# Kernel optimization log

Hardware: AMD Instinct MI355X
Metric: run time of the kernel (lower is better)

Reference implementation:

```python
import jax, jax.numpy as jnp
import numpy as np

# norse-default LIF/LI constants (RecNet overrides alpha=80, tau_mem_inv=100)
DT = 0.001
ALPHA = 80.0
TAU_SYN_INV = 200.0   # 1/5e-3 (default)
TAU_MEM_INV = 100.0   # 1/0.01 (passed explicitly)
V_TH, V_RESET, V_LEAK = 1.0, 0.0, 0.0

@jax.custom_vjp
def superspike(x):
    # heaviside forward, SuperSpike surrogate backward
    return (x > 0).astype(x.dtype)

def _ss_fwd(x):
    return (x > 0).astype(x.dtype), x

def _ss_bwd(x, g):
    return (g / (ALPHA * jnp.abs(x) + 1.0) ** 2,)

superspike.defvjp(_ss_fwd, _ss_bwd)

def setup_inputs() -> dict:
    key = jax.random.key(0)
    k1, k2, k3, k4 = jax.random.split(key, 4)
    T, B, F, H, O = 100, 512, 784, 512, 10
    x = jax.random.normal(k1, (T, B, 1, 28, 28), dtype=jnp.float32)
    w_in = jax.random.normal(k2, (H, F), dtype=jnp.float32) / np.sqrt(F)
    w_rec = jax.random.normal(k3, (H, H), dtype=jnp.float32) / np.sqrt(H)
    w_out = jax.random.normal(k4, (O, H), dtype=jnp.float32) / np.sqrt(H)
    return {"x": x, "w_in": w_in, "w_rec": w_rec, "w_out": w_out}

def reference(x, w_in, w_rec, w_out):
    T, B = x.shape[0], x.shape[1]
    Hd = w_in.shape[0]
    Od = w_out.shape[0]
    xf = x.reshape(T, B, -1)  # [T, B, F]

    z0 = jnp.zeros((B, Hd), x.dtype)
    lv0 = jnp.zeros((B, Od), x.dtype)
    init = (z0, z0, z0, lv0, lv0)  # (z, v, i, li_v, li_i)

    def step(carry, xt):
        z, v, i, lv, li = carry
        # LIF recurrent cell (norse lif_step)
        v_dec = v + DT * TAU_MEM_INV * ((V_LEAK - v) + i)
        i_dec = i - DT * TAU_SYN_INV * i
        z_new = superspike(v_dec - V_TH)
        v_new = (1.0 - z_new) * v_dec + z_new * V_RESET
        i_new = i_dec + xt @ w_in.T + z @ w_rec.T  # previous z for recurrence
        # readout linear (no bias)
        y = z_new @ w_out.T
        # LI cell (norse li_feed_forward_step): vo uses old current
        lv_new = lv + DT * TAU_MEM_INV * ((V_LEAK - lv) + li)
        li_new = li - DT * TAU_SYN_INV * li + y
        return (z_new, v_new, i_new, lv_new, li_new), lv_new

    _, voltages = jax.lax.scan(step, init, xf)
    return voltages  # [T, B, O]
```

## Files before the change

### kernel.cpp

```cpp
#include <hip/hip_runtime.h>


#define TT    100
#define BATCH 512
#define FDIM  784
#define HDIM  512
#define ODIM  10
#define NSTATE (BATCH * HDIM)

#define DTM 0.1
#define DTS 0.2

__global__ __launch_bounds__(256) void gemm_in_kernel(const float* __restrict__ A,
                                                      const float* __restrict__ B,
                                                      double* __restrict__ C) {
  __shared__ double As[16][130];
  __shared__ double Bs[16][66];
  const int tid = threadIdx.x;
  const int tn = tid & 15;
  const int tm = tid >> 4;
  const int m0 = blockIdx.x << 7;
  const int n0 = blockIdx.y << 6;

  double acc[8][4] = {};

  for (int kt = 0; kt < 49; ++kt) {
    __syncthreads();
#pragma unroll
    for (int s = 0; s < 2; ++s) {
      const int idx = tid + (s << 8);
      const int row = idx >> 2;
      const int kc  = (idx & 3) << 2;
      const float4 a = *(const float4*)(A + (size_t)(m0 + row) * FDIM + kt * 16 + kc);
      As[kc + 0][row] = (double)a.x; As[kc + 1][row] = (double)a.y;
      As[kc + 2][row] = (double)a.z; As[kc + 3][row] = (double)a.w;
    }
    {
      const int row = tid >> 2;
      const int kc  = (tid & 3) << 2;
      const float4 b = *(const float4*)(B + (size_t)(n0 + row) * FDIM + kt * 16 + kc);
      Bs[kc + 0][row] = (double)b.x; Bs[kc + 1][row] = (double)b.y;
      Bs[kc + 2][row] = (double)b.z; Bs[kc + 3][row] = (double)b.w;
    }
    __syncthreads();
#pragma unroll
    for (int kk = 0; kk < 16; ++kk) {
      double av[8], bv[4];
      *(double2*)&av[0] = *(const double2*)&As[kk][(tm << 3) + 0];
      *(double2*)&av[2] = *(const double2*)&As[kk][(tm << 3) + 2];
      *(double2*)&av[4] = *(const double2*)&As[kk][(tm << 3) + 4];
      *(double2*)&av[6] = *(const double2*)&As[kk][(tm << 3) + 6];
      *(double2*)&bv[0] = *(const double2*)&Bs[kk][(tn << 2) + 0];
      *(double2*)&bv[2] = *(const double2*)&Bs[kk][(tn << 2) + 2];
#pragma unroll
      for (int i = 0; i < 8; ++i)
#pragma unroll
        for (int j = 0; j < 4; ++j) acc[i][j] += av[i] * bv[j];
    }
  }
#pragma unroll
  for (int i = 0; i < 8; ++i) {
    double* crow = C + (size_t)(m0 + (tm << 3) + i) * HDIM + n0 + (tn << 2);
    *(double2*)(crow)     = make_double2(acc[i][0], acc[i][1]);
    *(double2*)(crow + 2) = make_double2(acc[i][2], acc[i][3]);
  }
}

__global__ __launch_bounds__(256) void transpose_kernel(const float* __restrict__ src,
                                                        float* __restrict__ dst) {
  __shared__ float tile[32][33];
  const int bx = blockIdx.x & 15, by = blockIdx.x >> 4;
  const int tx = threadIdx.x & 31, ty = threadIdx.x >> 5;
  const int x = (bx << 5) + tx;
#pragma unroll
  for (int s = 0; s < 32; s += 8)
    tile[ty + s][tx] = src[(size_t)((by << 5) + ty + s) * HDIM + x];
  __syncthreads();
  const int xo = (by << 5) + tx;
#pragma unroll
  for (int s = 0; s < 32; s += 8)
    dst[(size_t)((bx << 5) + ty + s) * HDIM + xo] = tile[tx][ty + s];
}

__global__ __launch_bounds__(256) void wot_kernel(const float* __restrict__ w_out,
                                                  float* __restrict__ wot) {
  const int k = (blockIdx.x << 8) + threadIdx.x;
#pragma unroll
  for (int o = 0; o < ODIM; ++o) wot[(k << 4) + o] = w_out[(size_t)o * HDIM + k];
}

__global__ __launch_bounds__(256) void lif_kernel(const double* __restrict__ cin,
                                                  const float* __restrict__ wrt,
                                                  const float* __restrict__ wot,
                                                  float* __restrict__ out) {
  const int b = blockIdx.x;
  const int tid = threadIdx.x;
  const int h0 = tid, h1 = tid + 256;

  __shared__ unsigned long long masks[8];
  __shared__ int offs[9];
  __shared__ __align__(8) unsigned short list[528];
  __shared__ double ypart[256];

  if (tid == 0) offs[8] = 0;
  __syncthreads();

  double v0 = 0.0, v1 = 0.0, i0 = 0.0, i1 = 0.0;
  double lv = 0.0, li = 0.0;

  const double* cinb = cin + (size_t)b * HDIM;
  float* outb = out + (size_t)b * ODIM;

  for (int t = 0; t < TT; ++t) {
    const double vd0 = v0 + DTM * ((0.0 - v0) + i0);
    const double vd1 = v1 + DTM * ((0.0 - v1) + i1);
    const bool s0 = (vd0 - 1.0) > 0.0;
    const bool s1 = (vd1 - 1.0) > 0.0;
    v0 = s0 ? 0.0 : vd0;
    v1 = s1 ? 0.0 : vd1;
    i0 = i0 - DTS * i0;
    i1 = i1 - DTS * i1;

    const double c0 = cinb[(size_t)t * NSTATE + h0];
    const double c1 = cinb[(size_t)t * NSTATE + h1];

    {
      const int nf = offs[8];
      const int nfp = (nf + 3) & ~3;
      if (nfp > 0) {
        float A0[4], A1[4], B0[4] = {}, B1[4] = {};
#define LOADG(base, X0, X1)                                                   \
        do {                                                                  \
          const unsigned long long le = *(const unsigned long long*)&list[base]; \
          const int k0 = (int)(le & 0xffffu), k1 = (int)((le >> 16) & 0xffffu); \
          const int k2 = (int)((le >> 32) & 0xffffu), k3 = (int)(le >> 48);   \
          X0[0] = wrt[(k0 << 9) + h0]; X1[0] = wrt[(k0 << 9) + h1];           \
          X0[1] = wrt[(k1 << 9) + h0]; X1[1] = wrt[(k1 << 9) + h1];           \
          X0[2] = wrt[(k2 << 9) + h0]; X1[2] = wrt[(k2 << 9) + h1];           \
          X0[3] = wrt[(k3 << 9) + h0]; X1[3] = wrt[(k3 << 9) + h1];           \
        } while (0)
        LOADG(0, A0, A1);
        for (int g = 0; g < nfp; g += 4) {
          if (g + 4 < nfp) LOADG(g + 4, B0, B1);
          i0 += (double)A0[0]; i1 += (double)A1[0];
          i0 += (double)A0[1]; i1 += (double)A1[1];
          i0 += (double)A0[2]; i1 += (double)A1[2];
          i0 += (double)A0[3]; i1 += (double)A1[3];
#pragma unroll
          for (int j = 0; j < 4; ++j) { A0[j] = B0[j]; A1[j] = B1[j]; }
        }
#undef LOADG
      }
    }
    i0 += c0;
    i1 += c1;

    __syncthreads();

    {
      const unsigned long long m0 = __ballot(s0);
      const unsigned long long m1 = __ballot(s1);
      const int w = tid >> 6;
      if ((tid & 63) == 0) { masks[w] = m0; masks[4 + w] = m1; }
    }
    __syncthreads();
    if (tid == 0) {
      int r = 0;
#pragma unroll
      for (int q = 0; q < 8; ++q) { offs[q] = r; r += __popcll(masks[q]); }
      offs[8] = r;
    }
    __syncthreads();
    if (tid < 8) {
      unsigned long long m = masks[tid];
      int o = offs[tid];
      const int base = tid << 6;
      while (m) {
        list[o++] = (unsigned short)(base + __builtin_ctzll(m));
        m &= m - 1;
      }
    }
    if (tid < 4) list[offs[8] + tid] = 512;
    __syncthreads();

    {
      const int o = tid & 15, q = tid >> 4;
      const int nfc = offs[8];
      double yp = 0.0;
      int kk = q;
      if (kk < nfc) {
        float f = wot[((int)list[kk] << 4) + o];
        for (kk += 16; kk < nfc; kk += 16) {
          const float fn = wot[((int)list[kk] << 4) + o];
          yp += (double)f;
          f = fn;
        }
        yp += (double)f;
      }
      ypart[(o << 4) + q] = yp;
    }
    __syncthreads();
    if (tid < ODIM) {
      double y = 0.0;
      const double* yr = &ypart[tid << 4];
#pragma unroll
      for (int q = 0; q < 16; ++q) y += yr[q];
      const double lvn = lv + DTM * ((0.0 - lv) + li);
      li = (li - DTS * li) + y;
      lv = lvn;
      outb[(size_t)t * (BATCH * ODIM) + tid] = (float)lvn;
    }
  }
}

extern "C" void kernel_launch(void* const* d_in, const int* in_sizes, int n_in,
                              void* d_out, int out_size, void* d_ws, size_t ws_size,
                              hipStream_t stream) {
  const float* x     = (const float*)d_in[0];
  const float* w_in  = (const float*)d_in[1];
  const float* w_rec = (const float*)d_in[2];
  const float* w_out = (const float*)d_in[3];
  float* out = (float*)d_out;

  const size_t CIN = (size_t)TT * BATCH * HDIM;
  double* cin = (double*)d_ws;
  float* wrt = (float*)(cin + CIN);
  float* wot = wrt + 513 * 512;

  const size_t aux_floats = 513ull * 512 + 513ull * 16;
  const size_t need_bytes = CIN * sizeof(double) + aux_floats * sizeof(float);
  if (ws_size < need_bytes) {
    hipMemsetAsync(d_out, 0x7F, (size_t)out_size * sizeof(float), stream);
    return;
  }

  hipMemsetAsync(wrt, 0, aux_floats * sizeof(float), stream);
  transpose_kernel<<<256, 256, 0, stream>>>(w_rec, wrt);
  wot_kernel<<<2, 256, 0, stream>>>(w_out, wot);
  gemm_in_kernel<<<dim3(400, 8), 256, 0, stream>>>(x, w_in, cin);
  lif_kernel<<<BATCH, 256, 0, stream>>>(cin, wrt, wot, out);
}
```

Baseline: 1.111 ms.

## Emulate FP64 input GEMM with int8 MFMA slice decomposition (Ozaki-style)

Replaces the scalar FP64 input-projection GEMM with an Ozaki-style scheme. Each row of x and w_in is split into five int8 slices under a shared per-row exponent, and the slice products are accumulated with int8 MFMA instructions. Only slice pairs above a significance cutoff are computed, then the partial sums are recombined into doubles. A small probe kernel first finds the MFMA lane layout at runtime, and the old FP64 path is kept as a fallback when the probe or workspace check fails. This trades extra slicing passes, workspace memory and truncated low-order bits for running the dominant GEMM on matrix cores.

Measured after the change: 1.634 ms. 1.47x slower.

```diff
diff --git a/kernel.cpp b/kernel.cpp
--- a/kernel.cpp
+++ b/kernel.cpp
@@ -7,62 +7,241 @@
 #define HDIM  512
 #define ODIM  10
 #define NSTATE (BATCH * HDIM)
+#define KPAD  832
 
 #define DTM 0.1
 #define DTS 0.2
 
-__global__ __launch_bounds__(256) void gemm_in_kernel(const float* __restrict__ A,
-                                                      const float* __restrict__ B,
-                                                      double* __restrict__ C) {
-  __shared__ double As[16][130];
-  __shared__ double Bs[16][66];
+typedef int i32x4 __attribute__((ext_vector_type(4)));
+
+__device__ __forceinline__ void h_maps(int H, int lane,
+                                       int& am, int& ak, int& bn, int& bk,
+                                       int dr[4], int dc[4]) {
+  const int l15 = lane & 15, l4 = lane >> 4;
+  const int lq = lane >> 2, l3 = lane & 3;
+  if (H & 1) { am = lq;  ak = l3; } else { am = l15; ak = l4; }
+  if (H & 2) { bn = lq;  bk = l3; } else { bn = l15; bk = l4; }
+  const int dmode = H >> 2;
+#pragma unroll
+  for (int r = 0; r < 4; ++r) {
+    const int rr = (dmode & 1) ? (l4 + (r << 2)) : ((l4 << 2) + r);
+    if (dmode & 2) { dr[r] = l15; dc[r] = rr; }
+    else           { dr[r] = rr;  dc[r] = l15; }
+  }
+}
+
+__device__ __forceinline__ int af_val(int m, int k, int s) {
+  return ((3 * m + 5 * k + 7 * s) % 11) - 5;
+}
+__device__ __forceinline__ int bf_val(int n, int k, int s) {
+  return ((2 * n + 7 * k + 3 * s) % 13) - 6;
+}
+
+__global__ __launch_bounds__(64) void probe_kernel(int* __restrict__ flag) {
+  const int lane = threadIdx.x;
+  int winner = -1;
+  for (int Hh = 0; Hh < 16; ++Hh) {
+    int am, ak, bn, bk, dr[4], dc[4];
+    h_maps(Hh, lane, am, ak, bn, bk, dr, dc);
+    bool ok = true;
+    for (int s = 0; s < 2; ++s) {
+      union { signed char c[16]; i32x4 v; } ua, ub;
+#pragma unroll
+      for (int j = 0; j < 16; ++j) {
+        ua.c[j] = (signed char)af_val(am, (ak << 4) + j, s);
+        ub.c[j] = (signed char)bf_val(bn, (bk << 4) + j, s);
+      }
+      i32x4 d = {0, 0, 0, 0};
+      d = __builtin_amdgcn_mfma_i32_16x16x64_i8(ua.v, ub.v, d, 0, 0, 0);
+#pragma unroll
+      for (int r = 0; r < 4; ++r) {
+        int ref = 0;
+        for (int k = 0; k < 64; ++k) ref += af_val(dr[r], k, s) * bf_val(dc[r], k, s);
+        ok = ok && (d[r] == ref);
+      }
+    }
+    if (__all(ok) && winner < 0) winner = Hh;
+  }
+  if (lane == 0) *flag = winner;
+}
+
+__global__ __launch_bounds__(256) void slice_kernel(const float* __restrict__ src,
+                                                    int rows,
+                                                    signed char* __restrict__ dst,
+                                                    int* __restrict__ Edst) {
+  const int w = (blockIdx.x << 2) + (threadIdx.x >> 6);
+  if (w >= rows) return;
+  const int lane = threadIdx.x & 63;
+  const float* rowp = src + (size_t)w * FDIM;
+  float vals[13];
+  float mx = 0.0f;
+#pragma unroll
+  for (int j = 0; j < 13; ++j) {
+    const int k = lane + (j << 6);
+    const float v = (k < FDIM) ? rowp[k] : 0.0f;
+    vals[j] = v;
+    mx = fmaxf(mx, fabsf(v));
+  }
+#pragma unroll
+  for (int o = 32; o; o >>= 1) mx = fmaxf(mx, __shfl_xor(mx, o));
+  const int E = (mx > 0.0f) ? (ilogbf(mx) + 3) : 3;
+  if (lane == 0) Edst[w] = E;
+#pragma unroll
+  for (int j = 0; j < 13; ++j) {
+    const int k = lane + (j << 6);
+    long long I = (long long)ldexp((double)vals[j], 40 - E);
+#pragma unroll
+    for (int s = 0; s < 5; ++s) {
+      int b = (int)(I & 255);
+      if (b > 127) { b -= 256; I += 256; }
+      I >>= 8;
+      dst[(size_t)s * rows * KPAD + (size_t)w * KPAD + k] = (signed char)b;
+    }
+  }
+}
+
+__global__ __launch_bounds__(256, 1) void gemm_in_kernel(
+    const float* __restrict__ A, const float* __restrict__ B,
+    const signed char* __restrict__ aslc, const signed char* __restrict__ bslc,
+    const int* __restrict__ Ea, const int* __restrict__ Eb,
+    double* __restrict__ C, const int* __restrict__ flag) {
+  __shared__ __align__(16) char smem[76800];
   const int tid = threadIdx.x;
-  const int tn = tid & 15;
-  const int tm = tid >> 4;
-  const int m0 = blockIdx.x << 7;
-  const int n0 = blockIdx.y << 6;
-
-  double acc[8][4] = {};
-
-  for (int kt = 0; kt < 49; ++kt) {
-    __syncthreads();
-#pragma unroll
-    for (int s = 0; s < 2; ++s) {
-      const int idx = tid + (s << 8);
-      const int row = idx >> 2;
-      const int kc  = (idx & 3) << 2;
-      const float4 a = *(const float4*)(A + (size_t)(m0 + row) * FDIM + kt * 16 + kc);
-      As[kc + 0][row] = (double)a.x; As[kc + 1][row] = (double)a.y;
-      As[kc + 2][row] = (double)a.z; As[kc + 3][row] = (double)a.w;
-    }
-    {
-      const int row = tid >> 2;
-      const int kc  = (tid & 3) << 2;
-      const float4 b = *(const float4*)(B + (size_t)(n0 + row) * FDIM + kt * 16 + kc);
-      Bs[kc + 0][row] = (double)b.x; Bs[kc + 1][row] = (double)b.y;
-      Bs[kc + 2][row] = (double)b.z; Bs[kc + 3][row] = (double)b.w;
-    }
-    __syncthreads();
-#pragma unroll
-    for (int kk = 0; kk < 16; ++kk) {
-      double av[8], bv[4];
-      *(double2*)&av[0] = *(const double2*)&As[kk][(tm << 3) + 0];
-      *(double2*)&av[2] = *(const double2*)&As[kk][(tm << 3) + 2];
-      *(double2*)&av[4] = *(const double2*)&As[kk][(tm << 3) + 4];
-      *(double2*)&av[6] = *(const double2*)&As[kk][(tm << 3) + 6];
-      *(double2*)&bv[0] = *(const double2*)&Bs[kk][(tn << 2) + 0];
-      *(double2*)&bv[2] = *(const double2*)&Bs[kk][(tn << 2) + 2];
-#pragma unroll
-      for (int i = 0; i < 8; ++i)
-#pragma unroll
-        for (int j = 0; j < 4; ++j) acc[i][j] += av[i] * bv[j];
-    }
-  }
-#pragma unroll
-  for (int i = 0; i < 8; ++i) {
-    double* crow = C + (size_t)(m0 + (tm << 3) + i) * HDIM + n0 + (tn << 2);
-    *(double2*)(crow)     = make_double2(acc[i][0], acc[i][1]);
-    *(double2*)(crow + 2) = make_double2(acc[i][2], acc[i][3]);
+  const int n0 = blockIdx.x << 6;
+  const int m0 = blockIdx.y << 7;
+  const int H = flag[0];
+
+  if (H >= 0) {
+    const int lane = tid & 63;
+    const int qm = (tid >> 6) & 1;
+    const int qn = tid >> 7;
+    int am, ak, bn, bk, dr[4], dc[4];
+    h_maps(H, lane, am, ak, bn, bk, dr, dc);
+    signed char* Ab = (signed char*)smem;
+    signed char* Bb = (signed char*)smem + 51200;
+
+    i32x4 acc[6][4][2];
+#pragma unroll
+    for (int gi = 0; gi < 6; ++gi)
+#pragma unroll
+      for (int mf = 0; mf < 4; ++mf)
+#pragma unroll
+        for (int nf = 0; nf < 2; ++nf) acc[gi][mf][nf] = (i32x4){0, 0, 0, 0};
+
+    for (int kt = 0; kt < 13; ++kt) {
+      __syncthreads();
+#pragma unroll
+      for (int it = 0; it < 15; ++it) {
+        const int c = tid + (it << 8);
+        const int4* gsrc;
+        char* ldst;
+        if (c < 2560) {
+          const int sa = c >> 9, rem = c & 511, row = rem >> 2, q = rem & 3;
+          gsrc = (const int4*)(aslc + (size_t)sa * (51200ull * KPAD)
+                               + (size_t)(m0 + row) * KPAD + kt * 64 + (q << 4));
+          ldst = (char*)(Ab + sa * 10240 + row * 80 + (q << 4));
+        } else {
+          const int c2 = c - 2560;
+          const int sb = c2 >> 8, rem = c2 & 255, row = rem >> 2, q = rem & 3;
+          gsrc = (const int4*)(bslc + (size_t)sb * (512ull * KPAD)
+                               + (size_t)(n0 + row) * KPAD + kt * 64 + (q << 4));
+          ldst = (char*)(Bb + sb * 5120 + row * 80 + (q << 4));
+        }
+        *(int4*)ldst = *gsrc;
+      }
+      __syncthreads();
+
+      i32x4 af[4][5], bf[2][5];
+#pragma unroll
+      for (int mf = 0; mf < 4; ++mf)
+#pragma unroll
+        for (int sa = 0; sa < 5; ++sa)
+          af[mf][sa] = *(const i32x4*)(Ab + sa * 10240
+                          + ((qm << 6) + (mf << 4) + am) * 80 + (ak << 4));
+#pragma unroll
+      for (int nf = 0; nf < 2; ++nf)
+#pragma unroll
+        for (int sb = 0; sb < 5; ++sb)
+          bf[nf][sb] = *(const i32x4*)(Bb + sb * 5120
+                          + ((qn << 5) + (nf << 4) + bn) * 80 + (bk << 4));
+#pragma unroll
+      for (int sa = 0; sa < 5; ++sa)
+#pragma unroll
+        for (int sb = 0; sb < 5; ++sb) {
+          if (sa + sb < 3) continue;
+          const int gi = sa + sb - 3;
+#pragma unroll
+          for (int mf = 0; mf < 4; ++mf)
+#pragma unroll
+            for (int nf = 0; nf < 2; ++nf)
+              acc[gi][mf][nf] = __builtin_amdgcn_mfma_i32_16x16x64_i8(
+                  af[mf][sa], bf[nf][sb], acc[gi][mf][nf], 0, 0, 0);
+        }
+    }
+
+#pragma unroll
+    for (int mf = 0; mf < 4; ++mf)
+#pragma unroll
+      for (int nf = 0; nf < 2; ++nf)
+#pragma unroll
+        for (int r = 0; r < 4; ++r) {
+          const int row = m0 + (qm << 6) + (mf << 4) + dr[r];
+          const int col = n0 + (qn << 5) + (nf << 4) + dc[r];
+          const int e0 = Ea[row] + Eb[col] - 80;
+          double s = 0.0;
+#pragma unroll
+          for (int g = 8; g >= 3; --g) {
+            const long long bits = ((long long)(e0 + 8 * g + 1023)) << 52;
+            s += (double)acc[g - 3][mf][nf][r] * __longlong_as_double(bits);
+          }
+          C[(size_t)row * HDIM + col] = s;
+        }
+  } else {
+    double (*As)[130] = (double(*)[130])smem;
+    double (*Bs)[66]  = (double(*)[66])(smem + 16640);
+    const int tn = tid & 15;
+    const int tm = tid >> 4;
+    double acc[8][4] = {};
+    for (int kt = 0; kt < 49; ++kt) {
+      __syncthreads();
+#pragma unroll
+      for (int s = 0; s < 2; ++s) {
+        const int idx = tid + (s << 8);
+        const int row = idx >> 2;
+        const int kc  = (idx & 3) << 2;
+        const float4 a = *(const float4*)(A + (size_t)(m0 + row) * FDIM + kt * 16 + kc);
+        As[kc + 0][row] = (double)a.x; As[kc + 1][row] = (double)a.y;
+        As[kc + 2][row] = (double)a.z; As[kc + 3][row] = (double)a.w;
+      }
+      {
+        const int row = tid >> 2;
+        const int kc  = (tid & 3) << 2;
+        const float4 b = *(const float4*)(B + (size_t)(n0 + row) * FDIM + kt * 16 + kc);
+        Bs[kc + 0][row] = (double)b.x; Bs[kc + 1][row] = (double)b.y;
+        Bs[kc + 2][row] = (double)b.z; Bs[kc + 3][row] = (double)b.w;
+      }
+      __syncthreads();
+#pragma unroll
+      for (int kk = 0; kk < 16; ++kk) {
+        double av[8], bv[4];
+        *(double2*)&av[0] = *(const double2*)&As[kk][(tm << 3) + 0];
+        *(double2*)&av[2] = *(const double2*)&As[kk][(tm << 3) + 2];
+        *(double2*)&av[4] = *(const double2*)&As[kk][(tm << 3) + 4];
+        *(double2*)&av[6] = *(const double2*)&As[kk][(tm << 3) + 6];
+        *(double2*)&bv[0] = *(const double2*)&Bs[kk][(tn << 2) + 0];
+        *(double2*)&bv[2] = *(const double2*)&Bs[kk][(tn << 2) + 2];
+#pragma unroll
+        for (int i = 0; i < 8; ++i)
+#pragma unroll
+          for (int j = 0; j < 4; ++j) acc[i][j] += av[i] * bv[j];
+      }
+    }
+#pragma unroll
+    for (int i = 0; i < 8; ++i) {
+      double* crow = C + (size_t)(m0 + (tm << 3) + i) * HDIM + n0 + (tn << 2);
+      *(double2*)(crow)     = make_double2(acc[i][0], acc[i][1]);
+      *(double2*)(crow + 2) = make_double2(acc[i][2], acc[i][3]);
+    }
   }
 }
 
@@ -165,10 +344,10 @@
     }
     __syncthreads();
     if (tid == 0) {
-      int r = 0;
-#pragma unroll
-      for (int q = 0; q < 8; ++q) { offs[q] = r; r += __popcll(masks[q]); }
-      offs[8] = r;
+      int rr = 0;
+#pragma unroll
+      for (int q = 0; q < 8; ++q) { offs[q] = rr; rr += __popcll(masks[q]); }
+      offs[8] = rr;
     }
     __syncthreads();
     if (tid < 8) {
@@ -224,19 +403,35 @@
 
   const size_t CIN = (size_t)TT * BATCH * HDIM;
   double* cin = (double*)d_ws;
-  float* wrt = (float*)(cin + CIN);
-  float* wot = wrt + 513 * 512;
-
-  const size_t aux_floats = 513ull * 512 + 513ull * 16;
-  const size_t need_bytes = CIN * sizeof(double) + aux_floats * sizeof(float);
-  if (ws_size < need_bytes) {
+  float* wrt  = (float*)(cin + CIN);
+  float* wot  = wrt + 513 * 512;
+  int*   flags = (int*)(wot + 513 * 16);
+  signed char* xslc = (signed char*)(flags + 4);
+  signed char* wslc = xslc + 5ull * 51200 * KPAD;
+  int* Ea = (int*)(wslc + 5ull * 512 * KPAD);
+  int* Eb = Ea + 51200;
+
+  const size_t zero_bytes = (513ull * 512 + 513ull * 16) * sizeof(float);
+  const size_t need_min = CIN * sizeof(double) + zero_bytes + 16;
+  const size_t need_i8  = need_min + 5ull * 51200 * KPAD + 5ull * 512 * KPAD
+                        + (51200ull + 512) * sizeof(int);
+  if (ws_size < need_min) {
     hipMemsetAsync(d_out, 0x7F, (size_t)out_size * sizeof(float), stream);
     return;
   }
-
-  hipMemsetAsync(wrt, 0, aux_floats * sizeof(float), stream);
+  const bool use_i8 = (ws_size >= need_i8);
+
+  hipMemsetAsync(wrt, 0, zero_bytes, stream);
+  if (use_i8) {
+    probe_kernel<<<1, 64, 0, stream>>>(flags);
+    slice_kernel<<<12800, 256, 0, stream>>>(x, 51200, xslc, Ea);
+    slice_kernel<<<128, 256, 0, stream>>>(w_in, 512, wslc, Eb);
+  } else {
+    hipMemsetAsync(flags, 0xFF, 4, stream);
+  }
   transpose_kernel<<<256, 256, 0, stream>>>(w_rec, wrt);
   wot_kernel<<<2, 256, 0, stream>>>(w_out, wot);
-  gemm_in_kernel<<<dim3(400, 8), 256, 0, stream>>>(x, w_in, cin);
+  gemm_in_kernel<<<dim3(8, 400), 256, 0, stream>>>(x, w_in, xslc, wslc, Ea, Eb,
+                                                   cin, flags);
   lif_kernel<<<BATCH, 256, 0, stream>>>(cin, wrt, wot, out);
 }
```
